# Kernel optimization log

Measured on AMD Instinct MI355X. Metric: run time of the kernel, lower is better.

The kernel has to match this reference:

```python
import jax, jax.numpy as jnp
import numpy as np

B, S, H = 2, 2048, 1024
E, K, I = 8, 2, 512
NSH = 2
IS = I * NSH           # shared-expert intermediate = moe_inter * n_shared_experts
NUM_TASKS = 3
TEMP = 1.0             # router_temperature_init (eval: no annealing, no noise)


def setup_inputs() -> dict:
    key = jax.random.key(0)
    ks = jax.random.split(key, 11)
    s_h = 1.0 / np.sqrt(H).astype(np.float32)
    s_i = 1.0 / np.sqrt(I).astype(np.float32)
    s_is = 1.0 / np.sqrt(IS).astype(np.float32)
    return {
        "hidden_states": jax.random.normal(ks[0], (B, S, H), jnp.float32),
        "task_id": 1,
        "gate_w": jax.random.normal(ks[1], (E, H), jnp.float32) * s_h,
        "task_emb": jax.random.normal(ks[2], (NUM_TASKS, H), jnp.float32) * 0.02,
        "We_gate": jax.random.normal(ks[3], (E, H, I), jnp.float32) * s_h,
        "We_up": jax.random.normal(ks[4], (E, H, I), jnp.float32) * s_h,
        "We_down": jax.random.normal(ks[5], (E, I, H), jnp.float32) * s_i,
        "Ws_gate": jax.random.normal(ks[6], (H, IS), jnp.float32) * s_h,
        "Ws_up": jax.random.normal(ks[7], (H, IS), jnp.float32) * s_h,
        "Ws_down": jax.random.normal(ks[8], (IS, H), jnp.float32) * s_is,
        "Wc": jax.random.normal(ks[9], (H, 2), jnp.float32) * s_h,
    }


def _gelu(x):
    return jax.nn.gelu(x, approximate=False)  # matches torch F.gelu default (erf)


def reference(hidden_states, task_id, gate_w, task_emb, We_gate, We_up, We_down,
              Ws_gate, Ws_up, Ws_down, Wc):
    b, s, h = hidden_states.shape
    flat = hidden_states.reshape(-1, h)            # [T, H]
    T = flat.shape[0]

    # ---- NoisyTopKGating (eval: no gumbel noise, no dropout, no aux loss) ----
    gate_in = flat + task_emb[task_id]             # task-conditioned router input
    logits = (gate_in @ gate_w.T) / TEMP           # [T, E]
    scores = jax.nn.softmax(logits, axis=-1)
    topk_w, topk_idx = jax.lax.top_k(scores, K)    # [T, K]
    topk_w = topk_w / (topk_w.sum(-1, keepdims=True) + 1e-20)  # norm_topk_prob

    # dense combine weights [T, E]: zero except the top-k routed experts
    w_dense = jnp.zeros((T, E), scores.dtype).at[
        jnp.arange(T)[:, None], topk_idx].set(topk_w)

    # ---- routed experts: gated MLP per expert, weighted scatter-combine ----
    g = _gelu(jnp.einsum('td,edi->eti', flat, We_gate))   # [E, T, I]
    u = jnp.einsum('td,edi->eti', flat, We_up)            # [E, T, I]
    local = jnp.einsum('eti,te,eid->td', g * u, w_dense, We_down)
    local = local.reshape(b, s, h)

    # ---- shared expert (wider gated MLP over all tokens) ----
    shared = (_gelu(hidden_states @ Ws_gate) * (hidden_states @ Ws_up)) @ Ws_down

    # ---- combination gate: softmax over (local, shared) ----
    alpha = jax.nn.softmax(hidden_states @ Wc, axis=-1)   # [B, S, 2]
    return alpha[..., 0:1] * local + alpha[..., 1:2] * shared
```

## Files before the change

### kernel.cpp

```cpp
#include <hip/hip_runtime.h>
#include <hip/hip_bf16.h>


typedef short  s16x8 __attribute__((ext_vector_type(8)));
typedef __bf16 bf16x8 __attribute__((ext_vector_type(8)));
typedef float  f32x4 __attribute__((ext_vector_type(4)));

__device__ __forceinline__ float b2f(ushort u) {
  union { unsigned int i; float f; } v; v.i = ((unsigned int)u) << 16; return v.f;
}
__device__ __forceinline__ ushort f2b(float f) {
  union { float f; unsigned int i; } v; v.f = f;
  unsigned int r = v.i + 0x7fffu + ((v.i >> 16) & 1u);
  return (ushort)(r >> 16);
}
__device__ __forceinline__ f32x4 mfma_bf16(s16x8 a, s16x8 b, f32x4 c) {
  return __builtin_amdgcn_mfma_f32_16x16x32_bf16(
      __builtin_bit_cast(bf16x8, a), __builtin_bit_cast(bf16x8, b), c, 0, 0, 0);
}
__device__ __forceinline__ void gll16(const ushort* g, const ushort* l) {
  __builtin_amdgcn_global_load_lds(
      (const __attribute__((address_space(1))) unsigned int*)g,
      (__attribute__((address_space(3))) unsigned int*)l, 16, 0, 0);
}

template<int MODE>
__global__ __launch_bounds__(256) void transpose_k(
    const float* __restrict__ S0, const float* __restrict__ S1,
    const float* __restrict__ S2, ushort* __restrict__ D0,
    ushort* __restrict__ D1, ushort* __restrict__ D2)
{
  const int z = blockIdx.z;
  const float* src; ushort* dst; int srcLd, dstLd;
  if (MODE == 0) {
    src = (z < 8 ? S0 + (size_t)z * 512 * 1024 : S1 + (size_t)(z - 8) * 512 * 1024);
    dst = (z < 8 ? D0 + (size_t)z * 512 * 1024 : D1 + (size_t)(z - 8) * 512 * 1024);
    srcLd = 512; dstLd = 1024;
  } else if (MODE == 1) {
    src = S0 + (size_t)z * 512 * 1024; dst = D0 + (size_t)z * 512;
    srcLd = 1024; dstLd = 5120;
  } else {
    src = (z == 0 ? S0 : z == 1 ? S1 : S2);
    dst = (z == 0 ? D0 : z == 1 ? D1 : D2);
    srcLd = 1024; dstLd = (z == 2 ? 5120 : 1024);
  }
  __shared__ float tile[32][33];
  const int c0 = blockIdx.x * 32, r0 = blockIdx.y * 32;
  const int tx = threadIdx.x & 31, ty = threadIdx.x >> 5;
#pragma unroll
  for (int j = 0; j < 4; ++j)
    tile[ty + j * 8][tx] = src[(size_t)(r0 + ty + j * 8) * srcLd + c0 + tx];
  __syncthreads();
#pragma unroll
  for (int j = 0; j < 4; ++j)
    dst[(size_t)(c0 + ty + j * 8) * dstLd + r0 + tx] = f2b(tile[tx][ty + j * 8]);
}

__global__ __launch_bounds__(256) void router_k(
    const float* __restrict__ X, const float* __restrict__ Gw,
    const float* __restrict__ Temb, const int* __restrict__ task_id,
    const float* __restrict__ Wc, float* __restrict__ scales,
    int* __restrict__ topk, ushort* __restrict__ Xb)
{
  const int wid = threadIdx.x >> 6, lane = threadIdx.x & 63;
  const int t = blockIdx.x * 4 + wid;
  const float* xr = X + t * 1024;
  const float* er = Temb + task_id[0] * 1024;

  float x[16], xe[16];
#pragma unroll
  for (int c = 0; c < 4; ++c) {
    float4 v = *(const float4*)&xr[c * 256 + lane * 4];
    float4 e = *(const float4*)&er[c * 256 + lane * 4];
    x[c * 4 + 0] = v.x; x[c * 4 + 1] = v.y; x[c * 4 + 2] = v.z; x[c * 4 + 3] = v.w;
    xe[c * 4 + 0] = v.x + e.x; xe[c * 4 + 1] = v.y + e.y;
    xe[c * 4 + 2] = v.z + e.z; xe[c * 4 + 3] = v.w + e.w;
  }
#pragma unroll
  for (int c = 0; c < 4; ++c) {
    ushort4 o;
    o.x = f2b(x[c * 4 + 0]); o.y = f2b(x[c * 4 + 1]);
    o.z = f2b(x[c * 4 + 2]); o.w = f2b(x[c * 4 + 3]);
    *(ushort4*)&Xb[t * 1024 + c * 256 + lane * 4] = o;
  }
  float logit[8];
#pragma unroll
  for (int e = 0; e < 8; ++e) {
    float p = 0.f;
#pragma unroll
    for (int c = 0; c < 4; ++c) {
      float4 g = *(const float4*)&Gw[e * 1024 + c * 256 + lane * 4];
      p += xe[c * 4] * g.x + xe[c * 4 + 1] * g.y + xe[c * 4 + 2] * g.z + xe[c * 4 + 3] * g.w;
    }
#pragma unroll
    for (int off = 32; off; off >>= 1) p += __shfl_xor(p, off);
    logit[e] = p;
  }
  float m = logit[0];
#pragma unroll
  for (int e = 1; e < 8; ++e) m = fmaxf(m, logit[e]);
  float pr[8], s = 0.f;
#pragma unroll
  for (int e = 0; e < 8; ++e) { pr[e] = expf(logit[e] - m); s += pr[e]; }
  float inv = 1.f / s;
#pragma unroll
  for (int e = 0; e < 8; ++e) pr[e] *= inv;
  int i1 = 0; float m1 = pr[0];
#pragma unroll
  for (int e = 1; e < 8; ++e) if (pr[e] > m1) { m1 = pr[e]; i1 = e; }
  int i2 = -1; float m2 = -1.f;
#pragma unroll
  for (int e = 0; e < 8; ++e) if (e != i1 && pr[e] > m2) { m2 = pr[e]; i2 = e; }
  float dn = 1.f / (m1 + m2 + 1e-20f);
  float w1 = m1 * dn, w2 = m2 * dn;

  float a0 = 0.f, a1 = 0.f;
#pragma unroll
  for (int c = 0; c < 4; ++c)
#pragma unroll
    for (int j = 0; j < 4; ++j) {
      int h = c * 256 + lane * 4 + j;
      a0 += x[c * 4 + j] * Wc[h * 2];
      a1 += x[c * 4 + j] * Wc[h * 2 + 1];
    }
#pragma unroll
  for (int off = 32; off; off >>= 1) {
    a0 += __shfl_xor(a0, off); a1 += __shfl_xor(a1, off);
  }
  float am = fmaxf(a0, a1);
  float ea0 = expf(a0 - am), ea1 = expf(a1 - am);
  float al0 = ea0 / (ea0 + ea1), al1 = ea1 / (ea0 + ea1);

  if (lane == 0) {
    scales[t * 4 + 0] = al0 * w1;
    scales[t * 4 + 1] = al0 * w2;
    scales[t * 4 + 2] = al1;
    topk[t * 2 + 0] = i1;
    topk[t * 2 + 1] = i2;
  }
}

__global__ __launch_bounds__(256) void indexbuild_k(
    const int* __restrict__ topk, const float* __restrict__ scales,
    int* __restrict__ tokmap, int* __restrict__ tokrows,
    float* __restrict__ rowscale, int* __restrict__ meta)
{
  __shared__ int cnt[8], cnt2[8], base[8];
  const int tid = threadIdx.x;
  if (tid < 8) { cnt[tid] = 0; cnt2[tid] = 0; }
  __syncthreads();
  for (int t = tid; t < 4096; t += 256) {
    atomicAdd(&cnt[topk[t * 2]], 1);
    atomicAdd(&cnt[topk[t * 2 + 1]], 1);
  }
  __syncthreads();
  if (tid == 0) {
    int nb = 0;
    for (int e = 0; e < 8; ++e) {
      base[e] = nb * 128;
      int blocks = (cnt[e] + 127) >> 7;
      for (int j = 0; j < blocks; ++j) meta[320 + nb + j] = e;
      nb += blocks;
    }
    meta[511] = nb;
  }
  __syncthreads();
  for (int t = tid; t < 4096; t += 256) {
#pragma unroll
    for (int r = 0; r < 2; ++r) {
      int e = topk[t * 2 + r];
      int slot = atomicAdd(&cnt2[e], 1);
      int row = base[e] + slot;
      tokmap[row] = t;
      rowscale[row] = scales[t * 4 + r];
      tokrows[t * 2 + r] = row;
    }
  }
  __syncthreads();
  for (int e = 0; e < 8; ++e) {
    int c = cnt[e], R = ((c + 127) >> 7) << 7;
    for (int j = c + tid; j < R; j += 256) {
      tokmap[base[e] + j] = 0;
      rowscale[base[e] + j] = 0.f;
    }
  }
}

__global__ __launch_bounds__(256) void gemm1_k(
    const ushort* __restrict__ Xb, const ushort* __restrict__ GT,
    const ushort* __restrict__ UT, const float* __restrict__ scales,
    const int* __restrict__ tokmap, const float* __restrict__ rowscale,
    const int* __restrict__ meta, ushort* __restrict__ Bg,
    ushort* __restrict__ Bs)
{
  __shared__ __align__(16) ushort lA[64 * 64];
  __shared__ __align__(16) ushort lG[64 * 64];
  __shared__ __align__(16) ushort lU[64 * 64];
  const int x = blockIdx.x, y = blockIdx.y;
  const bool routed = y < 144;
  if (routed && (x >= 8 || y >= 2 * meta[511])) return;

  const int tid = threadIdx.x, wid = tid >> 6, lane = tid & 63;
  const int col0 = x * 64;
  const int row0 = routed ? y * 64 : (y - 144) * 64;
  const int colG = routed ? (meta[320 + (y >> 1)] * 512 + col0) : (4096 + col0);
  const int wr = (wid >> 1) * 32, wc = (wid & 1) * 32;
  ushort* __restrict__ Out = routed ? Bg : Bs;
  const int outLd = routed ? 512 : 1024;

  int aOff[2], gOff[2], ldsO[2];
#pragma unroll
  for (int i = 0; i < 2; ++i) {
    int q = i * 256 + tid;
    int r = q >> 3, c = q & 7, lc = c ^ (r & 7);
    int arow = routed ? tokmap[row0 + r] : (row0 + r);
    aOff[i] = arow * 1024 + lc * 8;
    gOff[i] = (colG + r) * 1024 + lc * 8;
    ldsO[i] = (i * 256 + (tid & ~63)) * 8;
  }

  f32x4 accG[2][2] = {};
  f32x4 accU[2][2] = {};
  for (int k0 = 0; k0 < 1024; k0 += 64) {
    if (k0) __syncthreads();
#pragma unroll
    for (int i = 0; i < 2; ++i) gll16(Xb + aOff[i] + k0, lA + ldsO[i]);
#pragma unroll
    for (int i = 0; i < 2; ++i) gll16(GT + gOff[i] + k0, lG + ldsO[i]);
#pragma unroll
    for (int i = 0; i < 2; ++i) gll16(UT + gOff[i] + k0, lU + ldsO[i]);
    __syncthreads();
#pragma unroll
    for (int kc = 0; kc < 2; ++kc) {
      const int clog = kc * 4 + (lane >> 4);
      s16x8 af[2], gf[2], uf[2];
#pragma unroll
      for (int fr = 0; fr < 2; ++fr) {
        int rl = wr + fr * 16 + (lane & 15);
        af[fr] = *(const s16x8*)&lA[rl * 64 + ((clog ^ (rl & 7)) << 3)];
      }
#pragma unroll
      for (int cf = 0; cf < 2; ++cf) {
        int cl = wc + cf * 16 + (lane & 15);
        int off = cl * 64 + ((clog ^ (cl & 7)) << 3);
        gf[cf] = *(const s16x8*)&lG[off];
        uf[cf] = *(const s16x8*)&lU[off];
      }
#pragma unroll
      for (int fr = 0; fr < 2; ++fr)
#pragma unroll
        for (int cf = 0; cf < 2; ++cf) {
          accG[fr][cf] = mfma_bf16(af[fr], gf[cf], accG[fr][cf]);
          accU[fr][cf] = mfma_bf16(af[fr], uf[cf], accU[fr][cf]);
        }
    }
  }
#pragma unroll
  for (int fr = 0; fr < 2; ++fr)
#pragma unroll
    for (int r = 0; r < 4; ++r) {
      const int row = row0 + wr + fr * 16 + ((lane >> 4) << 2) + r;
      const float sc = routed ? rowscale[row] : scales[row * 4 + 2];
#pragma unroll
      for (int cf = 0; cf < 2; ++cf) {
        const int col = col0 + wc + cf * 16 + (lane & 15);
        float g = accG[fr][cf][r];
        float u = accU[fr][cf][r];
        float a = 0.5f * g * (1.0f + erff(g * 0.70710678118654752f));
        Out[(size_t)row * outLd + col] = f2b(a * u * sc);
      }
    }
}

template<int ROUTED>
__global__ __launch_bounds__(256) void gemm2_k(
    const ushort* __restrict__ A, const ushort* __restrict__ DT,
    const int* __restrict__ meta, const int* __restrict__ tokrows,
    const ushort* __restrict__ Rrows, ushort* __restrict__ OutB,
    float* __restrict__ OutF)
{
  __shared__ __align__(16) ushort lA[128 * 64];
  __shared__ __align__(16) ushort lB[128 * 64];
  int e = 0;
  if (ROUTED) {
    if ((int)blockIdx.y >= meta[511]) return;
    e = meta[320 + blockIdx.y];
  }
  const int K = ROUTED ? 512 : 1024;
  const int bBase = ROUTED ? e * 512 : 4096;
  const int tid = threadIdx.x, wid = tid >> 6, lane = tid & 63;
  const int col0 = blockIdx.x * 128, row0 = blockIdx.y * 128;
  const int wr = (wid >> 1) * 64, wc = (wid & 1) * 64;

  int aOff[4], bOff[4], lds[4];
#pragma unroll
  for (int i = 0; i < 4; ++i) {
    int q = i * 256 + tid;
    int r = q >> 3, c = q & 7, lc = c ^ (r & 7);
    aOff[i] = (row0 + r) * K + lc * 8;
    bOff[i] = (col0 + r) * 5120 + bBase + lc * 8;
    lds[i]  = (i * 256 + (tid & ~63)) * 8;
  }
  f32x4 acc[4][4] = {};
  for (int k0 = 0; k0 < K; k0 += 64) {
    if (k0) __syncthreads();
#pragma unroll
    for (int i = 0; i < 4; ++i) gll16(A + aOff[i] + k0, lA + lds[i]);
#pragma unroll
    for (int i = 0; i < 4; ++i) gll16(DT + bOff[i] + k0, lB + lds[i]);
    __syncthreads();
#pragma unroll
    for (int kc = 0; kc < 2; ++kc) {
      const int clog = kc * 4 + (lane >> 4);
      s16x8 af[4], bf[4];
#pragma unroll
      for (int fr = 0; fr < 4; ++fr) {
        int rl = wr + fr * 16 + (lane & 15);
        af[fr] = *(const s16x8*)&lA[rl * 64 + ((clog ^ (rl & 7)) << 3)];
      }
#pragma unroll
      for (int cf = 0; cf < 4; ++cf) {
        int cl = wc + cf * 16 + (lane & 15);
        bf[cf] = *(const s16x8*)&lB[cl * 64 + ((clog ^ (cl & 7)) << 3)];
      }
#pragma unroll
      for (int fr = 0; fr < 4; ++fr)
#pragma unroll
        for (int cf = 0; cf < 4; ++cf)
          acc[fr][cf] = mfma_bf16(af[fr], bf[cf], acc[fr][cf]);
    }
  }
#pragma unroll
  for (int fr = 0; fr < 4; ++fr)
#pragma unroll
    for (int r = 0; r < 4; ++r) {
      const int row = row0 + wr + fr * 16 + ((lane >> 4) << 2) + r;
      if (ROUTED) {
#pragma unroll
        for (int cf = 0; cf < 4; ++cf) {
          const int col = col0 + wc + cf * 16 + (lane & 15);
          OutB[row * 1024 + col] = f2b(acc[fr][cf][r]);
        }
      } else {
        const int r0 = tokrows[row * 2], r1 = tokrows[row * 2 + 1];
#pragma unroll
        for (int cf = 0; cf < 4; ++cf) {
          const int col = col0 + wc + cf * 16 + (lane & 15);
          float v = acc[fr][cf][r]
                  + b2f(Rrows[r0 * 1024 + col]) + b2f(Rrows[r1 * 1024 + col]);
          OutF[row * 1024 + col] = v;
        }
      }
    }
}

extern "C" void kernel_launch(void* const* d_in, const int* in_sizes, int n_in,
                              void* d_out, int out_size, void* d_ws, size_t ws_size,
                              hipStream_t stream) {
  const float* X    = (const float*)d_in[0];
  const int*   task = (const int*)  d_in[1];
  const float* Gw   = (const float*)d_in[2];
  const float* Temb = (const float*)d_in[3];
  const float* Weg  = (const float*)d_in[4];
  const float* Weu  = (const float*)d_in[5];
  const float* Wed  = (const float*)d_in[6];
  const float* Wsg  = (const float*)d_in[7];
  const float* Wsu  = (const float*)d_in[8];
  const float* Wsd  = (const float*)d_in[9];
  const float* Wc   = (const float*)d_in[10];

  char* ws = (char*)d_ws;
  float*  scales   = (float*)(ws + 0x00000);
  int*    topk     = (int*)  (ws + 0x10000);
  int*    tokmap   = (int*)  (ws + 0x18000);
  int*    tokrows  = (int*)  (ws + 0x22000);
  float*  rowscale = (float*)(ws + 0x2A000);
  int*    meta     = (int*)  (ws + 0x34000);
  ushort* Xb       = (ushort*)(ws + 0x40000);
  ushort* GT       = Xb + 4096 * 1024;
  ushort* UT       = GT + 5120 * 1024;
  ushort* DT       = UT + 5120 * 1024;
  ushort* Bg       = DT + 1024 * 5120;
  ushort* Bs       = Bg + 9216 * 512;
  ushort* out_r    = Bs + 4096 * 1024;

  transpose_k<0><<<dim3(16, 32, 16), 256, 0, stream>>>(Weg, Weu, nullptr, GT, UT, nullptr);
  transpose_k<1><<<dim3(32, 16, 8), 256, 0, stream>>>(Wed, nullptr, nullptr, DT, nullptr, nullptr);
  transpose_k<2><<<dim3(32, 32, 3), 256, 0, stream>>>(
      Wsg, Wsu, Wsd, GT + 4096 * 1024, UT + 4096 * 1024, DT + 4096);

  router_k<<<1024, 256, 0, stream>>>(X, Gw, Temb, task, Wc, scales, topk, Xb);
  indexbuild_k<<<1, 256, 0, stream>>>(topk, scales, tokmap, tokrows, rowscale, meta);

  gemm1_k<<<dim3(16, 208), 256, 0, stream>>>(Xb, GT, UT, scales, tokmap, rowscale, meta, Bg, Bs);

  gemm2_k<1><<<dim3(8, 72), 256, 0, stream>>>(Bg, DT, meta, tokrows, (const ushort*)nullptr, out_r, (float*)nullptr);
  gemm2_k<0><<<dim3(8, 32), 256, 0, stream>>>(Bs, DT, meta, tokrows, out_r, (ushort*)nullptr, (float*)d_out);
}
```

Before: 174.9 us.

## Fuse weight transposes and router into one prep kernel with vectorized tiles

The three weight-transpose launches and the router launch are merged into a single kernel. Block ID ranges select either a 64x64 transpose tile or router work. The transpose now loads float4 from global memory and writes 8 bf16 values (16 bytes) per store, where it previously used scalar accesses on 32x32 tiles. This removes three kernel launches and gaps, and widens the memory transactions of a bandwidth-bound conversion step. The cost is a 64x65 float shared tile for every block, including router blocks, which may lower occupancy.

```diff
diff --git a/kernel.cpp b/kernel.cpp
--- a/kernel.cpp
+++ b/kernel.cpp
@@ -24,46 +24,64 @@
       (__attribute__((address_space(3))) unsigned int*)l, 16, 0, 0);
 }
 
-template<int MODE>
-__global__ __launch_bounds__(256) void transpose_k(
-    const float* __restrict__ S0, const float* __restrict__ S1,
-    const float* __restrict__ S2, ushort* __restrict__ D0,
-    ushort* __restrict__ D1, ushort* __restrict__ D2)
-{
-  const int z = blockIdx.z;
-  const float* src; ushort* dst; int srcLd, dstLd;
-  if (MODE == 0) {
-    src = (z < 8 ? S0 + (size_t)z * 512 * 1024 : S1 + (size_t)(z - 8) * 512 * 1024);
-    dst = (z < 8 ? D0 + (size_t)z * 512 * 1024 : D1 + (size_t)(z - 8) * 512 * 1024);
-    srcLd = 512; dstLd = 1024;
-  } else if (MODE == 1) {
-    src = S0 + (size_t)z * 512 * 1024; dst = D0 + (size_t)z * 512;
-    srcLd = 1024; dstLd = 5120;
-  } else {
-    src = (z == 0 ? S0 : z == 1 ? S1 : S2);
-    dst = (z == 0 ? D0 : z == 1 ? D1 : D2);
-    srcLd = 1024; dstLd = (z == 2 ? 5120 : 1024);
-  }
-  __shared__ float tile[32][33];
-  const int c0 = blockIdx.x * 32, r0 = blockIdx.y * 32;
-  const int tx = threadIdx.x & 31, ty = threadIdx.x >> 5;
-#pragma unroll
-  for (int j = 0; j < 4; ++j)
-    tile[ty + j * 8][tx] = src[(size_t)(r0 + ty + j * 8) * srcLd + c0 + tx];
-  __syncthreads();
-#pragma unroll
-  for (int j = 0; j < 4; ++j)
-    dst[(size_t)(c0 + ty + j * 8) * dstLd + r0 + tx] = f2b(tile[tx][ty + j * 8]);
-}
-
-__global__ __launch_bounds__(256) void router_k(
+__global__ __launch_bounds__(256) void prep_k(
     const float* __restrict__ X, const float* __restrict__ Gw,
     const float* __restrict__ Temb, const int* __restrict__ task_id,
-    const float* __restrict__ Wc, float* __restrict__ scales,
-    int* __restrict__ topk, ushort* __restrict__ Xb)
+    const float* __restrict__ Wc,
+    const float* __restrict__ Weg, const float* __restrict__ Weu,
+    const float* __restrict__ Wed, const float* __restrict__ Wsg,
+    const float* __restrict__ Wsu, const float* __restrict__ Wsd,
+    ushort* __restrict__ GT, ushort* __restrict__ UT, ushort* __restrict__ DT,
+    float* __restrict__ scales, int* __restrict__ topk, ushort* __restrict__ Xb)
 {
-  const int wid = threadIdx.x >> 6, lane = threadIdx.x & 63;
-  const int t = blockIdx.x * 4 + wid;
+  __shared__ float tile[64][65];
+  const int id = blockIdx.x;
+  const int tid = threadIdx.x;
+
+  if (id < 3840) {
+    const float* src; ushort* dst; int srcLd, dstLd, r0, c0;
+    if (id < 2048) {
+      int z = id >> 7, rem = id & 127;
+      src = (z < 8) ? Weg + (size_t)z * 512 * 1024 : Weu + (size_t)(z - 8) * 512 * 1024;
+      dst = (z < 8) ? GT + (size_t)z * 512 * 1024 : UT + (size_t)(z - 8) * 512 * 1024;
+      srcLd = 512; dstLd = 1024;
+      r0 = (rem >> 3) * 64; c0 = (rem & 7) * 64;
+    } else if (id < 3072) {
+      int id2 = id - 2048, z = id2 >> 7, rem = id2 & 127;
+      src = Wed + (size_t)z * 512 * 1024; dst = DT + (size_t)z * 512;
+      srcLd = 1024; dstLd = 5120;
+      r0 = (rem & 7) * 64; c0 = (rem >> 3) * 64;
+    } else {
+      int id3 = id - 3072, z = id3 >> 8, rem = id3 & 255;
+      src = (z == 0 ? Wsg : z == 1 ? Wsu : Wsd);
+      dst = (z == 0 ? GT + 4096 * 1024 : z == 1 ? UT + 4096 * 1024 : DT + 4096);
+      srcLd = 1024; dstLd = (z == 2 ? 5120 : 1024);
+      r0 = (rem >> 4) * 64; c0 = (rem & 15) * 64;
+    }
+#pragma unroll
+    for (int it = 0; it < 4; ++it) {
+      int idx = it * 256 + tid;
+      int rr = idx >> 4, cc = (idx & 15) * 4;
+      float4 v = *(const float4*)&src[(size_t)(r0 + rr) * srcLd + c0 + cc];
+      tile[rr][cc] = v.x; tile[rr][cc + 1] = v.y;
+      tile[rr][cc + 2] = v.z; tile[rr][cc + 3] = v.w;
+    }
+    __syncthreads();
+#pragma unroll
+    for (int it = 0; it < 2; ++it) {
+      int idx = it * 256 + tid;
+      int c = idx >> 3, seg = (idx & 7) * 8;
+      s16x8 o;
+#pragma unroll
+      for (int j = 0; j < 8; ++j) o[j] = (short)f2b(tile[seg + j][c]);
+      *(s16x8*)&dst[(size_t)(c0 + c) * dstLd + r0 + seg] = o;
+    }
+    return;
+  }
+
+  const int rid = id - 3840;
+  const int wid = tid >> 6, lane = tid & 63;
+  const int t = rid * 4 + wid;
   const float* xr = X + t * 1024;
   const float* er = Temb + task_id[0] * 1024;
 
@@ -384,12 +402,9 @@
   ushort* Bs       = Bg + 9216 * 512;
   ushort* out_r    = Bs + 4096 * 1024;
 
-  transpose_k<0><<<dim3(16, 32, 16), 256, 0, stream>>>(Weg, Weu, nullptr, GT, UT, nullptr);
-  transpose_k<1><<<dim3(32, 16, 8), 256, 0, stream>>>(Wed, nullptr, nullptr, DT, nullptr, nullptr);
-  transpose_k<2><<<dim3(32, 32, 3), 256, 0, stream>>>(
-      Wsg, Wsu, Wsd, GT + 4096 * 1024, UT + 4096 * 1024, DT + 4096);
-
-  router_k<<<1024, 256, 0, stream>>>(X, Gw, Temb, task, Wc, scales, topk, Xb);
+  prep_k<<<4864, 256, 0, stream>>>(X, Gw, Temb, task, Wc,
+                                   Weg, Weu, Wed, Wsg, Wsu, Wsd,
+                                   GT, UT, DT, scales, topk, Xb);
   indexbuild_k<<<1, 256, 0, stream>>>(topk, scales, tokmap, tokrows, rowscale, meta);
 
   gemm1_k<<<dim3(16, 208), 256, 0, stream>>>(Xb, GT, UT, scales, tokmap, rowscale, meta, Bg, Bs);
```

Result: faster. 168.1 us (-3.9%).
